# Kernel tuning notes

Measured on AMD Instinct MI355X. Metric: run time of the kernel, lower is better.

Reference implementation:

```python
import jax, jax.numpy as jnp
import numpy as np

N, M, E = 100000, 500, 300000
XS, GS, OUT, HEADS = 100, 100, 100, 2
SLOPE = 0.2
EPS = 1e-12


def l2norm(x, axis):
    n = jnp.linalg.norm(x, axis=axis, keepdims=True)
    return x / jnp.maximum(n, EPS)


def gat_layer(h_ijk, ends, n, W, att):
    # W: [heads*out, in_dim] (no bias); att: [1, heads, out]
    heads, out = att.shape[1], att.shape[2]
    c = (h_ijk @ W.T).reshape(-1, heads, out)               # [E, H, D]
    a = jnp.sum(att * c, axis=2, keepdims=True)             # [E, H, 1]
    e = jnp.exp(-jax.nn.leaky_relu(a, SLOPE))
    denom = jax.ops.segment_sum(e, ends, num_segments=n)    # [n, H, 1]
    alpha = e / denom[ends]                                 # segment softmax (dropout=eval/identity)
    h = jax.ops.segment_sum(alpha * c, ends, num_segments=n)  # [n, H, D]
    h = jax.nn.elu(h)
    h = l2norm(h, axis=2)
    return h.reshape(n, heads * out)


def merge_layer(h_in, h_out, Wi, bi, Wo, bo, Wl, bl):
    hi = h_in @ Wi.T + bi
    ho = h_out @ Wo.T + bo
    lam = jax.nn.sigmoid(jnp.concatenate([hi, ho], axis=1) @ Wl.T + bl)
    h = lam * hi + (1.0 - lam) * ho
    return l2norm(jax.nn.elu(h), axis=1)


def setup_inputs() -> dict:
    key = jax.random.key(0)
    ks = jax.random.split(key, 24)
    D = HEADS * OUT  # 200
    in1 = 2 * XS + GS   # 300
    in2 = 3 * D         # 600
    s = 0.05
    return {
        'edge_idx': jax.random.randint(ks[0], (2, E), 0, N),
        'edge_type': jax.random.randint(ks[1], (E,), 0, M),
        'path_idx': jax.random.randint(ks[2], (2, 8), 0, N),
        'path_type': jax.random.randint(ks[3], (2, 8), 0, M),
        'use_path': 0,
        'x': jax.random.normal(ks[4], (N, XS), jnp.float32),
        'g': jax.random.normal(ks[5], (M, GS), jnp.float32),
        'W_in1': s * jax.random.normal(ks[6], (D, in1), jnp.float32),
        'att_in1': s * jax.random.normal(ks[7], (1, HEADS, OUT), jnp.float32),
        'W_out1': s * jax.random.normal(ks[8], (D, in1), jnp.float32),
        'att_out1': s * jax.random.normal(ks[9], (1, HEADS, OUT), jnp.float32),
        'Wi1': s * jax.random.normal(ks[10], (D, D), jnp.float32), 'bi1': jnp.zeros((D,), jnp.float32),
        'Wo1': s * jax.random.normal(ks[11], (D, D), jnp.float32), 'bo1': jnp.zeros((D,), jnp.float32),
        'Wl1': s * jax.random.normal(ks[12], (1, 2 * D), jnp.float32), 'bl1': jnp.zeros((1,), jnp.float32),
        'Wr': s * jax.random.normal(ks[13], (D, GS), jnp.float32), 'br': jnp.zeros((D,), jnp.float32),
        'Wf': s * jax.random.normal(ks[14], (D, in1), jnp.float32), 'bf': jnp.zeros((D,), jnp.float32),
        'W_in2': s * jax.random.normal(ks[15], (D, in2), jnp.float32),
        'att_in2': s * jax.random.normal(ks[16], (1, 1, D), jnp.float32),
        'W_out2': s * jax.random.normal(ks[17], (D, in2), jnp.float32),
        'att_out2': s * jax.random.normal(ks[18], (1, 1, D), jnp.float32),
        'Wi2': s * jax.random.normal(ks[19], (D, D), jnp.float32), 'bi2': jnp.zeros((D,), jnp.float32),
        'Wo2': s * jax.random.normal(ks[20], (D, D), jnp.float32), 'bo2': jnp.zeros((D,), jnp.float32),
        'Wl2': s * jax.random.normal(ks[21], (1, 2 * D), jnp.float32), 'bl2': jnp.zeros((1,), jnp.float32),
        'W_ent': s * jax.random.normal(ks[22], (D, XS), jnp.float32),
    }


def reference(edge_idx, edge_type, path_idx, path_type, use_path, x, g,
              W_in1, att_in1, W_out1, att_out1, Wi1, bi1, Wo1, bo1, Wl1, bl1,
              Wr, br, Wf, bf,
              W_in2, att_in2, W_out2, att_out2, Wi2, bi2, Wo2, bo2, Wl2, bl2,
              W_ent):
    n, m = x.shape[0], g.shape[0]
    x = l2norm(x, axis=1)  # x_initial is renormalized each forward
    row, col = edge_idx[0], edge_idx[1]
    # hop 1: gather-concat per-edge features [E, 2*XS+GS]
    h_ijk = jnp.concatenate([x[row], x[col], g[edge_type]], axis=1)
    h_in = gat_layer(h_ijk, col, n, W_in1, att_in1)
    h_out = gat_layer(h_ijk, row, n, W_out1, att_out1)
    h = merge_layer(h_in, h_out, Wi1, bi1, Wo1, bo1, Wl1, bl1)
    # relation layer
    g_edges = jax.ops.segment_sum(h_ijk, edge_type, num_segments=m)
    g_edges = jax.nn.elu(l2norm(g_edges, axis=1))
    g_prime = (g @ Wr.T + br) + (g_edges @ Wf.T + bf)
    # hop 2
    h_ijk2 = jnp.concatenate([h[row], h[col], g_prime[edge_type]], axis=1)
    h_in2 = gat_layer(h_ijk2, col, n, W_in2, att_in2)
    h_out2 = gat_layer(h_ijk2, row, n, W_out2, att_out2)
    h = merge_layer(h_in2, h_out2, Wi2, bi2, Wo2, bo2, Wl2, bl2)
    # entity residual layer
    h_prime = x @ W_ent.T + h
    return h_prime
```

## Files before the change

### kernel.cpp

```cpp
#include <hip/hip_runtime.h>
#include <cstddef>
#include <cstdint>

#define WSLOPE 0.2f
#define WEPS 1e-12f

typedef __attribute__((ext_vector_type(8))) short bf16x8;
typedef __attribute__((ext_vector_type(4))) float f32x4;

__device__ __forceinline__ float waveSum(float v) {
#pragma unroll
    for (int off = 32; off > 0; off >>= 1) v += __shfl_xor(v, off, 64);
    return v;
}
__device__ __forceinline__ float rowSum16(float v) {
#pragma unroll
    for (int off = 8; off > 0; off >>= 1) v += __shfl_xor(v, off, 64);
    return v;
}
__device__ __forceinline__ float eluf(float v) { return v > 0.f ? v : expm1f(v); }
__device__ __forceinline__ short f2bf(float f) {
    union { float f; uint32_t u; } v; v.f = f;
    uint32_t r = v.u + 0x7FFF + ((v.u >> 16) & 1);
    return (short)(r >> 16);
}
__device__ __forceinline__ float bf2f(short s) {
    union { uint32_t u; float f; } v; v.u = ((uint32_t)(uint16_t)s) << 16;
    return v.f;
}

__global__ void k_nodeprep(const float* __restrict__ x, float* __restrict__ invn,
                           short* __restrict__ xnb,
                           const float* __restrict__ wai, const float* __restrict__ wao,
                           float* __restrict__ rdi, float* __restrict__ cdi,
                           float* __restrict__ rdo, float* __restrict__ cdo, int N) {
    int wid = blockIdx.x * 4 + (threadIdx.x >> 6);
    int lane = threadIdx.x & 63;
    if (wid >= N) return;
    const float* p = x + (size_t)wid * 100;
    float a0 = p[lane];
    float a1 = (lane < 36) ? p[lane + 64] : 0.f;
    float ss = waveSum(a0 * a0 + a1 * a1);
    float inv = 1.f / fmaxf(sqrtf(ss), WEPS);
    if (lane == 0) invn[wid] = inv;
    float f0 = a0 * inv, f1 = a1 * inv;
    short* xb = xnb + (size_t)wid * 112;
    xb[lane] = f2bf(f0);
    if (lane < 36) xb[64 + lane] = f2bf(f1);
    else if (lane < 48) xb[64 + lane] = 0;
#pragma unroll
    for (int h = 0; h < 2; ++h) {
        const float* wi = wai + h * 300;
        const float* wo = wao + h * 300;
        float ri = f0 * wi[lane] + f1 * wi[lane + 64];
        float ci = f0 * wi[100 + lane] + f1 * wi[100 + lane + 64];
        float ro = f0 * wo[lane] + f1 * wo[lane + 64];
        float co = f0 * wo[100 + lane] + f1 * wo[100 + lane + 64];
        ri = waveSum(ri); ci = waveSum(ci); ro = waveSum(ro); co = waveSum(co);
        if (lane == 0) { rdi[wid * 2 + h] = ri; cdi[wid * 2 + h] = ci; rdo[wid * 2 + h] = ro; cdo[wid * 2 + h] = co; }
    }
}

__global__ void k_gprep(const float* __restrict__ g, short* __restrict__ gbf,
                        short* __restrict__ gcomb,
                        const float* __restrict__ wai, const float* __restrict__ wao,
                        float* __restrict__ gdi, float* __restrict__ gdo, int M) {
    int m = blockIdx.x * 4 + (threadIdx.x >> 6);
    int lane = threadIdx.x & 63;
    if (m >= M) return;
    const float* gm = g + (size_t)m * 100;
    float v0 = gm[lane];
    float v1 = (lane < 36) ? gm[lane + 64] : 0.f;
    short b0 = f2bf(v0), b1 = (lane < 36) ? f2bf(v1) : (short)0;
    short* gb = gbf + (size_t)m * 112;
    gb[lane] = b0;
    if (lane < 48) gb[64 + lane] = (lane < 36) ? b1 : (short)0;
    short* gc = gcomb + (size_t)m * 448;
    gc[lane] = b0;
    gc[64 + lane] = b1;
    float s0 = v0 * wai[200 + lane];
    float s1 = v0 * wai[500 + lane];
    float s2 = v0 * wao[200 + lane];
    float s3 = v0 * wao[500 + lane];
    if (lane < 36) {
        s0 += v1 * wai[264 + lane]; s1 += v1 * wai[564 + lane];
        s2 += v1 * wao[264 + lane]; s3 += v1 * wao[564 + lane];
    }
    s0 = waveSum(s0); s1 = waveSum(s1); s2 = waveSum(s2); s3 = waveSum(s3);
    if (lane == 0) { gdi[m * 2] = s0; gdi[m * 2 + 1] = s1; gdo[m * 2] = s2; gdo[m * 2 + 1] = s3; }
}

__global__ void k_count(const int* __restrict__ keys, int* __restrict__ cnt, int n) {
    int i = blockIdx.x * 256 + threadIdx.x;
    if (i < n) atomicAdd(&cnt[keys[i]], 1);
}

#define SCAN_CHUNK 2048
__global__ void k_blocksum(const int* __restrict__ cnt, int* __restrict__ bsum, int n) {
    __shared__ int sh[256];
    int b = blockIdx.x, t = threadIdx.x;
    int base = b * SCAN_CHUNK;
    int s = 0;
    for (int i = t; i < SCAN_CHUNK; i += 256) { int idx = base + i; if (idx < n) s += cnt[idx]; }
    sh[t] = s; __syncthreads();
    for (int off = 128; off > 0; off >>= 1) { if (t < off) sh[t] += sh[t + off]; __syncthreads(); }
    if (t == 0) bsum[b] = sh[0];
}

__global__ void k_scanwrite(const int* __restrict__ cnt, const int* __restrict__ bsum,
                            int* __restrict__ offs, int* __restrict__ cur, int n, int nb) {
    __shared__ int sh[256];
    __shared__ int sbase;
    int b = blockIdx.x, t = threadIdx.x;
    if (t == 0) { int s = 0; for (int i = 0; i < b; ++i) s += bsum[i]; sbase = s; }
    __syncthreads();
    int base = b * SCAN_CHUNK;
    int loc[8]; int ts = 0;
#pragma unroll
    for (int i = 0; i < 8; ++i) { int idx = base + t * 8 + i; int v = (idx < n) ? cnt[idx] : 0; loc[i] = ts; ts += v; }
    sh[t] = ts; __syncthreads();
    for (int off = 1; off < 256; off <<= 1) {
        int v = (t >= off) ? sh[t - off] : 0;
        __syncthreads();
        sh[t] += v;
        __syncthreads();
    }
    int excl = (t == 0) ? 0 : sh[t - 1];
    int gbase = sbase + excl;
#pragma unroll
    for (int i = 0; i < 8; ++i) {
        int idx = base + t * 8 + i;
        if (idx < n) { offs[idx] = gbase + loc[i]; cur[idx] = gbase + loc[i]; }
    }
    if (b == nb - 1 && t == 255) offs[n] = sbase + sh[255];
}

__global__ void k_scatter3(const int* __restrict__ keys, const int* __restrict__ other,
                           const int* __restrict__ et, int* __restrict__ cur,
                           int* __restrict__ nbrS, int* __restrict__ etS,
                           int* __restrict__ keyS, int n) {
    int i = blockIdx.x * 256 + threadIdx.x;
    if (i < n) {
        int p = atomicAdd(&cur[keys[i]], 1);
        nbrS[p] = other[i];
        etS[p] = et[i];
        keyS[p] = keys[i];
    }
}

__global__ void k_scatter2(const int* __restrict__ keys, int* __restrict__ cur,
                           int* __restrict__ rs, int* __restrict__ cs,
                           const int* __restrict__ row, const int* __restrict__ col, int n) {
    int i = blockIdx.x * 256 + threadIdx.x;
    if (i < n) {
        int p = atomicAdd(&cur[keys[i]], 1);
        rs[p] = row[i];
        cs[p] = col[i];
    }
}

__global__ void k_watt(const float* __restrict__ att, const float* __restrict__ W,
                       float* __restrict__ wa, int H, int DH, int K) {
    int id = blockIdx.x * 256 + threadIdx.x;
    if (id >= H * K) return;
    int h = id / K, k = id % K;
    float s = 0.f;
    for (int j = 0; j < DH; ++j) s += att[h * DH + j] * W[(size_t)(h * DH + j) * K + k];
    wa[id] = s;
}

__global__ void k_ew2(const int* __restrict__ nbi, const int* __restrict__ kyi,
                      const int* __restrict__ eti,
                      const int* __restrict__ nbo, const int* __restrict__ kyo,
                      const int* __restrict__ eto,
                      const float* __restrict__ rdi, const float* __restrict__ cdi,
                      const float* __restrict__ rdo, const float* __restrict__ cdo,
                      const float* __restrict__ gdi, const float* __restrict__ gdo,
                      float* __restrict__ ewi, float* __restrict__ ewo, int E, int H) {
    int id = blockIdx.x * 256 + threadIdx.x;
    int tot = E * H;
    if (id >= 2 * tot) return;
    if (id < tot) {
        int p = id / H, h = id - p * H;
        float a = rdi[nbi[p] * H + h] + cdi[kyi[p] * H + h] + gdi[eti[p] * H + h];
        float lr = a > 0.f ? a : WSLOPE * a;
        ewi[id] = expf(-lr);
    } else {
        int id2 = id - tot;
        int p = id2 / H, h = id2 - p * H;
        float a = cdo[nbo[p] * H + h] + rdo[kyo[p] * H + h] + gdo[eto[p] * H + h];
        float lr = a > 0.f ? a : WSLOPE * a;
        ewo[id2] = expf(-lr);
    }
}

template<bool HOP2>
__global__ void k_agg(const int* __restrict__ offs, const int* __restrict__ nbrS,
                      const int* __restrict__ etS, const float* __restrict__ ewS,
                      const short* __restrict__ featB, const short* __restrict__ gB,
                      short* __restrict__ A, int n0, int n1) {
    constexpr int H = HOP2 ? 1 : 2;
    constexpr int LDA = HOP2 ? 672 : 576;
    constexpr int FW = HOP2 ? 224 : 112;
    constexpr int GW = HOP2 ? 224 : 112;
    int node = n0 + blockIdx.x * 4 + (threadIdx.x >> 6);
    int lane = threadIdx.x & 63;
    if (node >= n1) return;
    int o = offs[node];
    int deg = offs[node + 1] - o;
    float va[7];
#pragma unroll
    for (int m = 0; m < 7; ++m) va[m] = 0.f;
    if (deg > 0) {
        float s0 = 0.f, s1 = 0.f;
        for (int i = lane; i < deg; i += 64) {
            s0 += ewS[(size_t)(o + i) * H];
            if (H == 2) s1 += ewS[(size_t)(o + i) * H + 1];
        }
        s0 = waveSum(s0);
        float rd0 = 1.f / s0, rd1 = rd0;
        if (H == 2) { s1 = waveSum(s1); rd1 = 1.f / s1; }
        for (int j = 0; j < deg; ++j) {
            float a0 = ewS[(size_t)(o + j) * H] * rd0;
            float a1 = (H == 2) ? ewS[(size_t)(o + j) * H + 1] * rd1 : a0;
            int nbr = nbrS[o + j];
            int et = etS[o + j];
            const short* fr = featB + (size_t)nbr * FW;
            const short* gr = gB + (size_t)et * GW;
            if (!HOP2) {
#pragma unroll
                for (int m = 0; m < 7; ++m) {
                    int d = lane + m * 64;
                    if (d < 100) va[m] += a0 * bf2f(fr[d]);
                    else if (d < 200) va[m] += a1 * bf2f(fr[d - 100]);
                    else if (d < 300) va[m] += a0 * bf2f(gr[d - 200]);
                    else if (d < 400) va[m] += a1 * bf2f(gr[d - 300]);
                }
            } else {
#pragma unroll
                for (int m = 0; m < 7; ++m) {
                    int d = lane + m * 64;
                    if (d < 200) va[m] += a0 * bf2f(fr[d]);
                    else if (d < 424) va[m] += a0 * bf2f(gr[d - 200]);
                }
            }
        }
    }
    size_t rb = (size_t)(node - n0);
    short* Ar = A + rb * LDA;
    if (!HOP2) {
#pragma unroll
        for (int m = 0; m < 7; ++m) {
            int d = lane + m * 64;
            if (d < 400) {
                int col = d < 100 ? d : (d < 200 ? d + 12 : (d < 300 ? d + 24 : d + 36));
                Ar[col] = f2bf(va[m]);
            }
        }
        if (lane < 48) { int q = lane / 12; int rm = lane - q * 12; Ar[q * 112 + 100 + rm] = 0; }
        const short* sf = featB + (size_t)node * 112;
#pragma unroll
        for (int mm = 0; mm < 2; ++mm) {
            int k = lane + mm * 64;
            if (k < 128) Ar[448 + k] = (deg > 0 && k < 112) ? sf[k] : (short)0;
        }
    } else {
#pragma unroll
        for (int m = 0; m < 7; ++m) {
            int d = lane + m * 64;
            if (d < 424) Ar[d < 200 ? d : d + 24] = f2bf(va[m]);
        }
        if (lane < 24) Ar[200 + lane] = 0;
        const short* sf = featB + (size_t)node * 224;
#pragma unroll
        for (int mm = 0; mm < 4; ++mm) {
            int k = lane + mm * 64;
            if (k < 224) Ar[448 + k] = deg > 0 ? sf[k] : (short)0;
        }
    }
}

template<int KSTEPS, int H>
__launch_bounds__(256)
__global__ void k_mgemm_post(const short* __restrict__ A, const short* __restrict__ Wb,
                             short* __restrict__ post, int rows, int lda) {
    constexpr int LDW = KSTEPS * 32;
    const int t = threadIdx.x;
    const int wv = t >> 6, l = t & 63;
    const int lhi = l >> 4, llo = l & 15;
    const int rbase = blockIdx.x * 64 + wv * 16;
    f32x4 acc[13];
#pragma unroll
    for (int j = 0; j < 13; ++j) acc[j] = f32x4{0.f, 0.f, 0.f, 0.f};
    const short* arow = A + (size_t)(rbase + llo) * lda + lhi * 8;
#pragma unroll
    for (int kt = 0; kt < KSTEPS; ++kt) {
        bf16x8 a = *(const bf16x8*)(arow + kt * 32);
#pragma unroll
        for (int j = 0; j < 13; ++j) {
            bf16x8 b = *(const bf16x8*)(Wb + (size_t)(j * 16 + llo) * LDW + kt * 32 + lhi * 8);
            acc[j] = __builtin_amdgcn_mfma_f32_16x16x32_bf16(a, b, acc[j], 0, 0, 0);
        }
    }
    const int r0 = rbase + lhi * 4;
#pragma unroll
    for (int e = 0; e < 4; ++e) {
        int r = r0 + e;
        if (r >= rows) continue;
        float v[13];
        float s0 = 0.f, s1 = 0.f;
#pragma unroll
        for (int j = 0; j < 13; ++j) {
            int d = j * 16 + llo;
            if (d < 200) {
                float xv = eluf(acc[j][e]);
                v[j] = xv;
                if (H == 1 || d < 100) s0 += xv * xv; else s1 += xv * xv;
            }
        }
        s0 = rowSum16(s0);
        float inv0 = 1.f / fmaxf(sqrtf(s0), WEPS);
        float inv1 = inv0;
        if (H == 2) { s1 = rowSum16(s1); inv1 = 1.f / fmaxf(sqrtf(s1), WEPS); }
        short* pr = post + (size_t)r * 224;
#pragma unroll
        for (int j = 0; j < 13; ++j) {
            int d = j * 16 + llo;
            if (d < 200) pr[d] = f2bf(v[j] * ((H == 2 && d >= 100) ? inv1 : inv0));
        }
    }
}

template<bool HOP1>
__launch_bounds__(512)
__global__ void k_mergemm2(const short* __restrict__ pA, const short* __restrict__ pB,
                           const short* __restrict__ Wi, const short* __restrict__ Wo,
                           const float* __restrict__ bi, const float* __restrict__ bo,
                           const float* __restrict__ Wl, const float* __restrict__ bl,
                           const short* __restrict__ xnb, const short* __restrict__ Went,
                           float* __restrict__ outf, short* __restrict__ h1b,
                           const float* __restrict__ wa2i, const float* __restrict__ wa2o,
                           float* __restrict__ rdi, float* __restrict__ cdi,
                           float* __restrict__ rdo, float* __restrict__ cdo,
                           int rows) {
    __shared__ float lpS[2][64];
    __shared__ float ssS[2][64];
    __shared__ float dotS[2][64][4];
    const int t = threadIdx.x;
    const int wvAll = t >> 6;
    const int rg = wvAll >> 1;
    const int half = wvAll & 1;
    const int l = t & 63;
    const int lhi = l >> 4, llo = l & 15;
    const int jbase = half * 7;
    const int rbase = blockIdx.x * 64 + rg * 16;
    f32x4 accA[7], accB[7];
#pragma unroll
    for (int j = 0; j < 7; ++j) { accA[j] = f32x4{0.f, 0.f, 0.f, 0.f}; accB[j] = f32x4{0.f, 0.f, 0.f, 0.f}; }
    const short* pa = pA + (size_t)(rbase + llo) * 224 + lhi * 8;
    const short* pb = pB + (size_t)(rbase + llo) * 224 + lhi * 8;
#pragma unroll
    for (int kt = 0; kt < 7; ++kt) {
        bf16x8 a1 = *(const bf16x8*)(pa + kt * 32);
        bf16x8 a2 = *(const bf16x8*)(pb + kt * 32);
#pragma unroll
        for (int j = 0; j < 7; ++j) {
            if (jbase + j < 13) {
                bf16x8 b1 = *(const bf16x8*)(Wi + (size_t)((jbase + j) * 16 + llo) * 224 + kt * 32 + lhi * 8);
                accA[j] = __builtin_amdgcn_mfma_f32_16x16x32_bf16(a1, b1, accA[j], 0, 0, 0);
                bf16x8 b2 = *(const bf16x8*)(Wo + (size_t)((jbase + j) * 16 + llo) * 224 + kt * 32 + lhi * 8);
                accB[j] = __builtin_amdgcn_mfma_f32_16x16x32_bf16(a2, b2, accB[j], 0, 0, 0);
            }
        }
    }
    f32x4 accR[7];
    if (!HOP1) {
#pragma unroll
        for (int j = 0; j < 7; ++j) accR[j] = f32x4{0.f, 0.f, 0.f, 0.f};
        const short* xr = xnb + (size_t)(rbase + llo) * 112 + lhi * 8;
#pragma unroll
        for (int kt = 0; kt < 4; ++kt) {
            bf16x8 a = *(const bf16x8*)(xr + kt * 32);
#pragma unroll
            for (int j = 0; j < 7; ++j) {
                if (jbase + j < 13) {
                    bf16x8 b = *(const bf16x8*)(Went + (size_t)((jbase + j) * 16 + llo) * 128 + kt * 32 + lhi * 8);
                    accR[j] = __builtin_amdgcn_mfma_f32_16x16x32_bf16(a, b, accR[j], 0, 0, 0);
                }
            }
        }
    }
    const int r0 = rbase + lhi * 4;
    const int rrb = rg * 16 + lhi * 4;
    float blv = bl[0];
#pragma unroll
    for (int e = 0; e < 4; ++e) {
        float lp = 0.f;
#pragma unroll
        for (int j = 0; j < 7; ++j) {
            int d = (jbase + j) * 16 + llo;
            if (jbase + j < 13 && d < 200)
                lp += Wl[d] * (accA[j][e] + bi[d]) + Wl[200 + d] * (accB[j][e] + bo[d]);
        }
        lp = rowSum16(lp);
        if (llo == 0) lpS[half][rrb + e] = lp;
    }
    __syncthreads();
    float lamAll[4];
#pragma unroll
    for (int e = 0; e < 4; ++e) {
        float lam = 1.f / (1.f + expf(-(lpS[0][rrb + e] + lpS[1][rrb + e] + blv)));
        lamAll[e] = lam;
        float ss = 0.f;
#pragma unroll
        for (int j = 0; j < 7; ++j) {
            int d = (jbase + j) * 16 + llo;
            if (jbase + j < 13 && d < 200) {
                float vi = accA[j][e] + bi[d];
                float vo = accB[j][e] + bo[d];
                float hv = eluf(lam * vi + (1.f - lam) * vo);
                ss += hv * hv;
            }
        }
        ss = rowSum16(ss);
        if (llo == 0) ssS[half][rrb + e] = ss;
    }
    __syncthreads();
#pragma unroll
    for (int e = 0; e < 4; ++e) {
        int r = r0 + e;
        if (r >= rows) continue;
        float inv = 1.f / fmaxf(sqrtf(ssS[0][rrb + e] + ssS[1][rrb + e]), WEPS);
        float lam = lamAll[e];
        float ri = 0.f, ci = 0.f, ro = 0.f, co = 0.f;
#pragma unroll
        for (int j = 0; j < 7; ++j) {
            if (jbase + j >= 13) continue;
            int d = (jbase + j) * 16 + llo;
            if (d < 200) {
                float vi = accA[j][e] + bi[d];
                float vo = accB[j][e] + bo[d];
                float val = eluf(lam * vi + (1.f - lam) * vo) * inv;
                if (HOP1) {
                    h1b[(size_t)r * 224 + d] = f2bf(val);
                    ri += val * wa2i[d]; ci += val * wa2i[200 + d];
                    ro += val * wa2o[d]; co += val * wa2o[200 + d];
                } else {
                    outf[(size_t)r * 200 + d] = val + accR[j][e];
                }
            } else if (HOP1) {
                h1b[(size_t)r * 224 + d] = 0;
            }
        }
        if (HOP1) {
            if (half) h1b[(size_t)r * 224 + 208 + llo] = 0;
            ri = rowSum16(ri); ci = rowSum16(ci); ro = rowSum16(ro); co = rowSum16(co);
            if (llo == 0) {
                dotS[half][rrb + e][0] = ri; dotS[half][rrb + e][1] = ci;
                dotS[half][rrb + e][2] = ro; dotS[half][rrb + e][3] = co;
            }
        }
    }
    if (HOP1) {
        __syncthreads();
        if (half == 0 && llo == 0) {
#pragma unroll
            for (int e = 0; e < 4; ++e) {
                int r = r0 + e;
                if (r < rows) {
                    rdi[r] = dotS[0][rrb + e][0] + dotS[1][rrb + e][0];
                    cdi[r] = dotS[0][rrb + e][1] + dotS[1][rrb + e][1];
                    rdo[r] = dotS[0][rrb + e][2] + dotS[1][rrb + e][2];
                    cdo[r] = dotS[0][rrb + e][3] + dotS[1][rrb + e][3];
                }
            }
        }
    }
}

__launch_bounds__(256)
__global__ void k_mgemm_rel(const short* __restrict__ A, const short* __restrict__ Wb,
                            const float* __restrict__ brf,
                            short* __restrict__ gout, const float* __restrict__ wai,
                            const float* __restrict__ wao,
                            float* __restrict__ gdi, float* __restrict__ gdo, int rows) {
    constexpr int KSTEPS = 14, LDW = KSTEPS * 32;
    const int t = threadIdx.x;
    const int wv = t >> 6, l = t & 63;
    const int lhi = l >> 4, llo = l & 15;
    const int rbase = blockIdx.x * 64 + wv * 16;
    f32x4 acc[13];
#pragma unroll
    for (int j = 0; j < 13; ++j) acc[j] = f32x4{0.f, 0.f, 0.f, 0.f};
    const short* arow = A + (size_t)(rbase + llo) * 448 + lhi * 8;
#pragma unroll
    for (int kt = 0; kt < KSTEPS; ++kt) {
        bf16x8 a = *(const bf16x8*)(arow + kt * 32);
#pragma unroll
        for (int j = 0; j < 13; ++j) {
            bf16x8 b = *(const bf16x8*)(Wb + (size_t)(j * 16 + llo) * LDW + kt * 32 + lhi * 8);
            acc[j] = __builtin_amdgcn_mfma_f32_16x16x32_bf16(a, b, acc[j], 0, 0, 0);
        }
    }
    const int r0 = rbase + lhi * 4;
#pragma unroll
    for (int e = 0; e < 4; ++e) {
        int r = r0 + e;
        if (r >= rows) continue;
        short* pr = gout + (size_t)r * 224;
        float gi = 0.f, go = 0.f;
#pragma unroll
        for (int j = 0; j < 13; ++j) {
            int d = j * 16 + llo;
            if (d < 200) {
                float val = acc[j][e] + brf[d];
                pr[d] = f2bf(val);
                gi += val * wai[400 + d];
                go += val * wao[400 + d];
            } else {
                pr[d] = 0;
            }
        }
        pr[208 + llo] = 0;
        gi = rowSum16(gi); go = rowSum16(go);
        if (llo == 0) { gdi[r] = gi; gdo[r] = go; }
    }
}

__global__ void k_prepw(const float* __restrict__ W, int ldW, int koff, int Klen, int span,
                        int mode, short* __restrict__ Wb, int ldWb, int dst) {
    int id = blockIdx.x * 256 + threadIdx.x;
    int tot = 208 * span;
    if (id >= tot) return;
    int d = id / span, k = id - d * span;
    float v = 0.f;
    if (d < 200) {
        if (mode == 0) { if (k < Klen) v = W[(size_t)d * ldW + koff + k]; }
        else { int h = d / 100; int kk = k - h * 112; if (kk >= 0 && kk < Klen) v = W[(size_t)d * ldW + koff + kk]; }
    }
    Wb[(size_t)d * ldWb + dst + k] = f2bf(v);
}

__global__ void k_prepwrf(const float* __restrict__ Wr, const float* __restrict__ Wf,
                          short* __restrict__ Wb) {
    int id = blockIdx.x * 256 + threadIdx.x;
    if (id >= 208 * 448) return;
    int d = id / 448, k = id - d * 448;
    float v = 0.f;
    if (d < 200) {
        if (k < 100) v = Wr[(size_t)d * 100 + k];
        else if (k >= 128 && k < 428) v = Wf[(size_t)d * 300 + (k - 128)];
    }
    Wb[id] = f2bf(v);
}

__global__ void k_brf(const float* __restrict__ br, const float* __restrict__ bf,
                      float* __restrict__ brf) {
    int d = threadIdx.x;
    if (d < 200) brf[d] = br[d] + bf[d];
}

__global__ void k_gedges_b(const int* __restrict__ rsT, const int* __restrict__ csT,
                           const int* __restrict__ offsT,
                           const float* __restrict__ x, const float* __restrict__ invn,
                           const float* __restrict__ g, short* __restrict__ gcomb, int M) {
    __shared__ float red[6];
    int m = blockIdx.x, t = threadIdx.x;
    int o = offsT[m];
    int deg = offsT[m + 1] - o;
    float acc = 0.f;
    if (t < 128) {
        int d = t; bool ok = d < 100;
        for (int i = 0; i < deg; ++i) {
            int r = rsT[o + i];
            if (ok) acc += x[(size_t)r * 100 + d] * invn[r];
        }
    } else if (t < 256) {
        int d = t - 128; bool ok = d < 100;
        for (int i = 0; i < deg; ++i) {
            int c = csT[o + i];
            if (ok) acc += x[(size_t)c * 100 + d] * invn[c];
        }
    } else {
        int d = t - 256;
        if (d < 100) acc = (float)deg * g[(size_t)m * 100 + d];
    }
    float sq = waveSum(acc * acc);
    if ((t & 63) == 0) red[t >> 6] = sq;
    __syncthreads();
    float s2 = red[0] + red[1] + red[2] + red[3] + red[4] + red[5];
    float inv = 1.f / fmaxf(sqrtf(s2), WEPS);
    short* orow = gcomb + (size_t)m * 448 + 128;
    if (t < 128) {
        if (t < 100) orow[t] = f2bf(eluf(acc * inv));
    } else if (t < 256) {
        int d = t - 128;
        if (d < 100) orow[100 + d] = f2bf(eluf(acc * inv));
    } else {
        int d = t - 256;
        if (d < 100) orow[200 + d] = f2bf(eluf(acc * inv));
        else if (d < 120) orow[200 + d] = 0;
    }
}

extern "C" void kernel_launch(void* const* d_in, const int* in_sizes, int n_in,
                              void* d_out, int out_size, void* d_ws, size_t ws_size,
                              hipStream_t stream) {
    const int* eidx   = (const int*)d_in[0];
    const int* etype  = (const int*)d_in[1];
    const float* x    = (const float*)d_in[5];
    const float* g    = (const float*)d_in[6];
    const float* W_in1  = (const float*)d_in[7];
    const float* att_in1 = (const float*)d_in[8];
    const float* W_out1 = (const float*)d_in[9];
    const float* att_out1 = (const float*)d_in[10];
    const float* Wi1 = (const float*)d_in[11]; const float* bi1 = (const float*)d_in[12];
    const float* Wo1 = (const float*)d_in[13]; const float* bo1 = (const float*)d_in[14];
    const float* Wl1 = (const float*)d_in[15]; const float* bl1 = (const float*)d_in[16];
    const float* Wr  = (const float*)d_in[17]; const float* br  = (const float*)d_in[18];
    const float* Wf  = (const float*)d_in[19]; const float* bf  = (const float*)d_in[20];
    const float* W_in2  = (const float*)d_in[21]; const float* att_in2 = (const float*)d_in[22];
    const float* W_out2 = (const float*)d_in[23]; const float* att_out2 = (const float*)d_in[24];
    const float* Wi2 = (const float*)d_in[25]; const float* bi2 = (const float*)d_in[26];
    const float* Wo2 = (const float*)d_in[27]; const float* bo2 = (const float*)d_in[28];
    const float* Wl2 = (const float*)d_in[29]; const float* bl2 = (const float*)d_in[30];
    const float* W_ent = (const float*)d_in[31];

    const int E = in_sizes[1];
    const int N = in_sizes[5] / 100;
    const int M = in_sizes[6] / 100;
    const int Mr = (M + 63) & ~63;
    float* out = (float*)d_out;
    const int* row = eidx;
    const int* col = eidx + E;

    char* w = (char*)d_ws;
    size_t off_b = 0;
    auto alloc = [&](size_t bytes) -> void* {
        void* p = w + off_b;
        off_b += (bytes + 255) & ~(size_t)255;
        return p;
    };
    float* invn  = (float*)alloc((size_t)N * 4);
    short* h1_bf = (short*)alloc((size_t)(N + 64) * 224 * 2);
    short* xn_bf = (short*)alloc((size_t)(N + 64) * 112 * 2);
    short* g_bf  = (short*)alloc((size_t)M * 112 * 2);
    short* gp_bf = (short*)alloc((size_t)Mr * 224 * 2);
    int* offs_in = (int*)alloc((size_t)(N + 1) * 4);
    int* offs_out= (int*)alloc((size_t)(N + 1) * 4);
    int* offsT   = (int*)alloc((size_t)(M + 1) * 4);
    int* nbrS_in = (int*)alloc((size_t)E * 4);
    int* etS_in  = (int*)alloc((size_t)E * 4);
    int* keyS_in = (int*)alloc((size_t)E * 4);
    int* nbrS_out= (int*)alloc((size_t)E * 4);
    int* etS_out = (int*)alloc((size_t)E * 4);
    int* keyS_out= (int*)alloc((size_t)E * 4);
    int* rsT     = (int*)alloc((size_t)E * 4);
    int* csT     = (int*)alloc((size_t)E * 4);
    int* cnt     = (int*)alloc((size_t)N * 4);
    int* cur     = (int*)alloc((size_t)N * 4);
    int* bsum    = (int*)alloc((size_t)64 * 4);
    float* wa1_in = (float*)alloc((size_t)640 * 4);
    float* wa1_out= (float*)alloc((size_t)640 * 4);
    float* wa2_in = (float*)alloc((size_t)640 * 4);
    float* wa2_out= (float*)alloc((size_t)640 * 4);
    float* rdot_in = (float*)alloc((size_t)N * 2 * 4);
    float* cdot_in = (float*)alloc((size_t)N * 2 * 4);
    float* rdot_out= (float*)alloc((size_t)N * 2 * 4);
    float* cdot_out= (float*)alloc((size_t)N * 2 * 4);
    float* gdot_in = (float*)alloc((size_t)M * 2 * 4);
    float* gdot_out= (float*)alloc((size_t)M * 2 * 4);
    float* ewS_in  = (float*)alloc((size_t)E * 2 * 4);
    float* ewS_out = (float*)alloc((size_t)E * 2 * 4);
    short* gcomb   = (short*)alloc((size_t)Mr * 448 * 2);
    short* Wc_in1  = (short*)alloc((size_t)208 * 576 * 2);
    short* Wc_out1 = (short*)alloc((size_t)208 * 576 * 2);
    short* Wc_in2  = (short*)alloc((size_t)208 * 672 * 2);
    short* Wc_out2 = (short*)alloc((size_t)208 * 672 * 2);
    short* Wm_i1   = (short*)alloc((size_t)208 * 224 * 2);
    short* Wm_o1   = (short*)alloc((size_t)208 * 224 * 2);
    short* Wm_i2   = (short*)alloc((size_t)208 * 224 * 2);
    short* Wm_o2   = (short*)alloc((size_t)208 * 224 * 2);
    short* Wb_ent  = (short*)alloc((size_t)208 * 128 * 2);
    short* Wrf_b   = (short*)alloc((size_t)208 * 448 * 2);
    float* brf     = (float*)alloc((size_t)200 * 4);

    if (off_b >= ws_size) return;
    size_t rem = ws_size - off_b;
    long long Cll = (long long)(rem / 3712);
    long long Nr64 = ((long long)N + 63) & ~63LL;
    int C = (int)(Cll > Nr64 ? Nr64 : Cll);
    C &= ~63;
    if (C < 64) return;
    short* Ac0   = (short*)alloc((size_t)C * 672 * 2);
    short* Ac1   = (short*)alloc((size_t)C * 672 * 2);
    short* postA = (short*)alloc((size_t)C * 224 * 2);
    short* postB = (short*)alloc((size_t)C * 224 * 2);
    if (off_b > ws_size) return;

    const int gE = (E + 255) / 256;
    const int gN4 = (N + 3) / 4;
    const int gM4 = (M + 3) / 4;
    const int gM64 = (M + 63) / 64;

    hipMemsetAsync(postA, 0, (size_t)C * 224 * 2, stream);
    hipMemsetAsync(postB, 0, (size_t)C * 224 * 2, stream);

    auto gsp = [](int span) { return (208 * span + 255) / 256; };
    k_prepw<<<gsp(224), 256, 0, stream>>>(W_in1, 300, 0, 100, 224, 1, Wc_in1, 576, 0);
    k_prepw<<<gsp(224), 256, 0, stream>>>(W_in1, 300, 200, 100, 224, 1, Wc_in1, 576, 224);
    k_prepw<<<gsp(128), 256, 0, stream>>>(W_in1, 300, 100, 100, 128, 0, Wc_in1, 576, 448);
    k_prepw<<<gsp(224), 256, 0, stream>>>(W_out1, 300, 100, 100, 224, 1, Wc_out1, 576, 0);
    k_prepw<<<gsp(224), 256, 0, stream>>>(W_out1, 300, 200, 100, 224, 1, Wc_out1, 576, 224);
    k_prepw<<<gsp(128), 256, 0, stream>>>(W_out1, 300, 0, 100, 128, 0, Wc_out1, 576, 448);
    k_prepw<<<gsp(224), 256, 0, stream>>>(W_in2, 600, 0, 200, 224, 0, Wc_in2, 672, 0);
    k_prepw<<<gsp(224), 256, 0, stream>>>(W_in2, 600, 400, 200, 224, 0, Wc_in2, 672, 224);
    k_prepw<<<gsp(224), 256, 0, stream>>>(W_in2, 600, 200, 200, 224, 0, Wc_in2, 672, 448);
    k_prepw<<<gsp(224), 256, 0, stream>>>(W_out2, 600, 200, 200, 224, 0, Wc_out2, 672, 0);
    k_prepw<<<gsp(224), 256, 0, stream>>>(W_out2, 600, 400, 200, 224, 0, Wc_out2, 672, 224);
    k_prepw<<<gsp(224), 256, 0, stream>>>(W_out2, 600, 0, 200, 224, 0, Wc_out2, 672, 448);
    k_prepw<<<gsp(224), 256, 0, stream>>>(Wi1, 200, 0, 200, 224, 0, Wm_i1, 224, 0);
    k_prepw<<<gsp(224), 256, 0, stream>>>(Wo1, 200, 0, 200, 224, 0, Wm_o1, 224, 0);
    k_prepw<<<gsp(224), 256, 0, stream>>>(Wi2, 200, 0, 200, 224, 0, Wm_i2, 224, 0);
    k_prepw<<<gsp(224), 256, 0, stream>>>(Wo2, 200, 0, 200, 224, 0, Wm_o2, 224, 0);
    k_prepw<<<gsp(128), 256, 0, stream>>>(W_ent, 100, 0, 100, 128, 0, Wb_ent, 128, 0);
    k_prepwrf<<<gsp(448), 256, 0, stream>>>(Wr, Wf, Wrf_b);
    k_brf<<<1, 256, 0, stream>>>(br, bf, brf);

    int nbN = (N + SCAN_CHUNK - 1) / SCAN_CHUNK;
    int nbM = (M + SCAN_CHUNK - 1) / SCAN_CHUNK;
    hipMemsetAsync(cnt, 0, (size_t)N * 4, stream);
    k_count<<<gE, 256, 0, stream>>>(col, cnt, E);
    k_blocksum<<<nbN, 256, 0, stream>>>(cnt, bsum, N);
    k_scanwrite<<<nbN, 256, 0, stream>>>(cnt, bsum, offs_in, cur, N, nbN);
    k_scatter3<<<gE, 256, 0, stream>>>(col, row, etype, cur, nbrS_in, etS_in, keyS_in, E);

    hipMemsetAsync(cnt, 0, (size_t)N * 4, stream);
    k_count<<<gE, 256, 0, stream>>>(row, cnt, E);
    k_blocksum<<<nbN, 256, 0, stream>>>(cnt, bsum, N);
    k_scanwrite<<<nbN, 256, 0, stream>>>(cnt, bsum, offs_out, cur, N, nbN);
    k_scatter3<<<gE, 256, 0, stream>>>(row, col, etype, cur, nbrS_out, etS_out, keyS_out, E);

    hipMemsetAsync(cnt, 0, (size_t)M * 4, stream);
    k_count<<<gE, 256, 0, stream>>>(etype, cnt, E);
    k_blocksum<<<nbM, 256, 0, stream>>>(cnt, bsum, M);
    k_scanwrite<<<nbM, 256, 0, stream>>>(cnt, bsum, offsT, cur, M, nbM);
    k_scatter2<<<gE, 256, 0, stream>>>(etype, cur, rsT, csT, row, col, E);

    k_watt<<<(600 + 255) / 256, 256, 0, stream>>>(att_in1, W_in1, wa1_in, 2, 100, 300);
    k_watt<<<(600 + 255) / 256, 256, 0, stream>>>(att_out1, W_out1, wa1_out, 2, 100, 300);
    k_watt<<<(600 + 255) / 256, 256, 0, stream>>>(att_in2, W_in2, wa2_in, 1, 200, 600);
    k_watt<<<(600 + 255) / 256, 256, 0, stream>>>(att_out2, W_out2, wa2_out, 1, 200, 600);

    k_nodeprep<<<gN4, 256, 0, stream>>>(x, invn, xn_bf, wa1_in, wa1_out,
                                        rdot_in, cdot_in, rdot_out, cdot_out, N);
    k_gprep<<<gM4, 256, 0, stream>>>(g, g_bf, gcomb, wa1_in, wa1_out, gdot_in, gdot_out, M);
    k_ew2<<<(2 * E * 2 + 255) / 256, 256, 0, stream>>>(nbrS_in, keyS_in, etS_in,
                                                       nbrS_out, keyS_out, etS_out,
                                                       rdot_in, cdot_in, rdot_out, cdot_out,
                                                       gdot_in, gdot_out, ewS_in, ewS_out, E, 2);

    for (int n0 = 0; n0 < N; n0 += C) {
        int rows = (N - n0 < C) ? (N - n0) : C;
        int n1 = n0 + rows;
        int ga = (rows + 3) / 4;
        int gb = (rows + 63) / 64;
        k_agg<false><<<ga, 256, 0, stream>>>(offs_in, nbrS_in, etS_in, ewS_in, xn_bf, g_bf, Ac0, n0, n1);
        k_agg<false><<<ga, 256, 0, stream>>>(offs_out, nbrS_out, etS_out, ewS_out, xn_bf, g_bf, Ac1, n0, n1);
        k_mgemm_post<18, 2><<<gb, 256, 0, stream>>>(Ac0, Wc_in1, postA, rows, 576);
        k_mgemm_post<18, 2><<<gb, 256, 0, stream>>>(Ac1, Wc_out1, postB, rows, 576);
        k_mergemm2<true><<<gb, 512, 0, stream>>>(postA, postB, Wm_i1, Wm_o1, bi1, bo1, Wl1, bl1,
                                                 nullptr, nullptr,
                                                 nullptr, h1_bf + (size_t)n0 * 224,
                                                 wa2_in, wa2_out,
                                                 rdot_in + n0, cdot_in + n0,
                                                 rdot_out + n0, cdot_out + n0, rows);
    }

    k_gedges_b<<<M, 384, 0, stream>>>(rsT, csT, offsT, x, invn, g, gcomb, M);
    k_mgemm_rel<<<gM64, 256, 0, stream>>>(gcomb, Wrf_b, brf, gp_bf, wa2_in, wa2_out, gdot_in, gdot_out, M);

    k_ew2<<<(2 * E + 255) / 256, 256, 0, stream>>>(nbrS_in, keyS_in, etS_in,
                                                   nbrS_out, keyS_out, etS_out,
                                                   rdot_in, cdot_in, rdot_out, cdot_out,
                                                   gdot_in, gdot_out, ewS_in, ewS_out, E, 1);

    for (int n0 = 0; n0 < N; n0 += C) {
        int rows = (N - n0 < C) ? (N - n0) : C;
        int n1 = n0 + rows;
        int ga = (rows + 3) / 4;
        int gb = (rows + 63) / 64;
        k_agg<true><<<ga, 256, 0, stream>>>(offs_in, nbrS_in, etS_in, ewS_in, h1_bf, gp_bf, Ac0, n0, n1);
        k_agg<true><<<ga, 256, 0, stream>>>(offs_out, nbrS_out, etS_out, ewS_out, h1_bf, gp_bf, Ac1, n0, n1);
        k_mgemm_post<21, 1><<<gb, 256, 0, stream>>>(Ac0, Wc_in2, postA, rows, 672);
        k_mgemm_post<21, 1><<<gb, 256, 0, stream>>>(Ac1, Wc_out2, postB, rows, 672);
        k_mergemm2<false><<<gb, 512, 0, stream>>>(postA, postB, Wm_i2, Wm_o2, bi2, bo2, Wl2, bl2,
                                                  xn_bf + (size_t)n0 * 112, Wb_ent,
                                                  out + (size_t)n0 * 200, nullptr,
                                                  nullptr, nullptr,
                                                  nullptr, nullptr, nullptr, nullptr, rows);
    }
}
```

Baseline: 2.535 ms.

## Read self features directly in GEMM instead of copying into staging buffer

```diff
diff --git a/kernel.cpp b/kernel.cpp
--- a/kernel.cpp
+++ b/kernel.cpp
@@ -75,9 +75,9 @@
     short* gb = gbf + (size_t)m * 112;
     gb[lane] = b0;
     if (lane < 48) gb[64 + lane] = (lane < 36) ? b1 : (short)0;
-    short* gc = gcomb + (size_t)m * 448;
+    short* gc = gcomb + (size_t)m * 416;
     gc[lane] = b0;
-    gc[64 + lane] = b1;
+    if (lane < 48) gc[64 + lane] = (lane < 36) ? b1 : (short)0;
     float s0 = v0 * wai[200 + lane];
     float s1 = v0 * wai[500 + lane];
     float s2 = v0 * wao[200 + lane];
@@ -200,7 +200,7 @@
                       const short* __restrict__ featB, const short* __restrict__ gB,
                       short* __restrict__ A, int n0, int n1) {
     constexpr int H = HOP2 ? 1 : 2;
-    constexpr int LDA = HOP2 ? 672 : 576;
+    constexpr int LDA = 448;
     constexpr int FW = HOP2 ? 224 : 112;
     constexpr int GW = HOP2 ? 224 : 112;
     int node = n0 + blockIdx.x * 4 + (threadIdx.x >> 6);
@@ -258,12 +258,6 @@
             }
         }
         if (lane < 48) { int q = lane / 12; int rm = lane - q * 12; Ar[q * 112 + 100 + rm] = 0; }
-        const short* sf = featB + (size_t)node * 112;
-#pragma unroll
-        for (int mm = 0; mm < 2; ++mm) {
-            int k = lane + mm * 64;
-            if (k < 128) Ar[448 + k] = (deg > 0 && k < 112) ? sf[k] : (short)0;
-        }
     } else {
 #pragma unroll
         for (int m = 0; m < 7; ++m) {
@@ -271,34 +265,45 @@
             if (d < 424) Ar[d < 200 ? d : d + 24] = f2bf(va[m]);
         }
         if (lane < 24) Ar[200 + lane] = 0;
-        const short* sf = featB + (size_t)node * 224;
-#pragma unroll
-        for (int mm = 0; mm < 4; ++mm) {
-            int k = lane + mm * 64;
-            if (k < 224) Ar[448 + k] = deg > 0 ? sf[k] : (short)0;
-        }
-    }
-}
-
-template<int KSTEPS, int H>
+    }
+}
+
+template<int KS_S, int H>
 __launch_bounds__(256)
 __global__ void k_mgemm_post(const short* __restrict__ A, const short* __restrict__ Wb,
-                             short* __restrict__ post, int rows, int lda) {
-    constexpr int LDW = KSTEPS * 32;
+                             const short* __restrict__ selfB, int selfLD,
+                             const int* __restrict__ offs,
+                             short* __restrict__ post, int rows) {
+    constexpr int KS_A = 14;
+    constexpr int LDW = (KS_A + KS_S) * 32;
     const int t = threadIdx.x;
     const int wv = t >> 6, l = t & 63;
     const int lhi = l >> 4, llo = l & 15;
     const int rbase = blockIdx.x * 64 + wv * 16;
+    const int ra = rbase + llo;
+    const int deg = (ra < rows) ? (offs[ra + 1] - offs[ra]) : 0;
     f32x4 acc[13];
 #pragma unroll
     for (int j = 0; j < 13; ++j) acc[j] = f32x4{0.f, 0.f, 0.f, 0.f};
-    const short* arow = A + (size_t)(rbase + llo) * lda + lhi * 8;
-#pragma unroll
-    for (int kt = 0; kt < KSTEPS; ++kt) {
+    const short* arow = A + (size_t)ra * 448 + lhi * 8;
+#pragma unroll
+    for (int kt = 0; kt < KS_A; ++kt) {
         bf16x8 a = *(const bf16x8*)(arow + kt * 32);
 #pragma unroll
         for (int j = 0; j < 13; ++j) {
             bf16x8 b = *(const bf16x8*)(Wb + (size_t)(j * 16 + llo) * LDW + kt * 32 + lhi * 8);
+            acc[j] = __builtin_amdgcn_mfma_f32_16x16x32_bf16(a, b, acc[j], 0, 0, 0);
+        }
+    }
+    const short* srow = selfB + (size_t)ra * selfLD + lhi * 8;
+#pragma unroll
+    for (int kt = 0; kt < KS_S; ++kt) {
+        bf16x8 a;
+        if (deg > 0) a = *(const bf16x8*)(srow + kt * 32);
+        else a = bf16x8{0, 0, 0, 0, 0, 0, 0, 0};
+#pragma unroll
+        for (int j = 0; j < 13; ++j) {
+            bf16x8 b = *(const bf16x8*)(Wb + (size_t)(j * 16 + llo) * LDW + (KS_A + kt) * 32 + lhi * 8);
             acc[j] = __builtin_amdgcn_mfma_f32_16x16x32_bf16(a, b, acc[j], 0, 0, 0);
         }
     }
@@ -484,7 +489,7 @@
                             short* __restrict__ gout, const float* __restrict__ wai,
                             const float* __restrict__ wao,
                             float* __restrict__ gdi, float* __restrict__ gdo, int rows) {
-    constexpr int KSTEPS = 14, LDW = KSTEPS * 32;
+    constexpr int KSTEPS = 13, LDW = KSTEPS * 32;
     const int t = threadIdx.x;
     const int wv = t >> 6, l = t & 63;
     const int lhi = l >> 4, llo = l & 15;
@@ -492,7 +497,7 @@
     f32x4 acc[13];
 #pragma unroll
     for (int j = 0; j < 13; ++j) acc[j] = f32x4{0.f, 0.f, 0.f, 0.f};
-    const short* arow = A + (size_t)(rbase + llo) * 448 + lhi * 8;
+    const short* arow = A + (size_t)(rbase + llo) * 416 + lhi * 8;
 #pragma unroll
     for (int kt = 0; kt < KSTEPS; ++kt) {
         bf16x8 a = *(const bf16x8*)(arow + kt * 32);
@@ -544,12 +549,12 @@
 __global__ void k_prepwrf(const float* __restrict__ Wr, const float* __restrict__ Wf,
                           short* __restrict__ Wb) {
     int id = blockIdx.x * 256 + threadIdx.x;
-    if (id >= 208 * 448) return;
-    int d = id / 448, k = id - d * 448;
+    if (id >= 208 * 416) return;
+    int d = id / 416, k = id - d * 416;
     float v = 0.f;
     if (d < 200) {
         if (k < 100) v = Wr[(size_t)d * 100 + k];
-        else if (k >= 128 && k < 428) v = Wf[(size_t)d * 300 + (k - 128)];
+        else if (k >= 112 && k < 412) v = Wf[(size_t)d * 300 + (k - 112)];
     }
     Wb[id] = f2bf(v);
 }
@@ -563,7 +568,7 @@
 __global__ void k_gedges_b(const int* __restrict__ rsT, const int* __restrict__ csT,
                            const int* __restrict__ offsT,
                            const float* __restrict__ x, const float* __restrict__ invn,
-                           const float* __restrict__ g, short* __restrict__ gcomb, int M) {
+                           const short* __restrict__ gbf, short* __restrict__ gcomb, int M) {
     __shared__ float red[6];
     int m = blockIdx.x, t = threadIdx.x;
     int o = offsT[m];
@@ -583,14 +588,14 @@
         }
     } else {
         int d = t - 256;
-        if (d < 100) acc = (float)deg * g[(size_t)m * 100 + d];
+        if (d < 100) acc = (float)deg * bf2f(gbf[(size_t)m * 112 + d]);
     }
     float sq = waveSum(acc * acc);
     if ((t & 63) == 0) red[t >> 6] = sq;
     __syncthreads();
     float s2 = red[0] + red[1] + red[2] + red[3] + red[4] + red[5];
     float inv = 1.f / fmaxf(sqrtf(s2), WEPS);
-    short* orow = gcomb + (size_t)m * 448 + 128;
+    short* orow = gcomb + (size_t)m * 416 + 112;
     if (t < 128) {
         if (t < 100) orow[t] = f2bf(eluf(acc * inv));
     } else if (t < 256) {
@@ -599,7 +604,7 @@
     } else {
         int d = t - 256;
         if (d < 100) orow[200 + d] = f2bf(eluf(acc * inv));
-        else if (d < 120) orow[200 + d] = 0;
+        else if (d < 104) orow[200 + d] = 0;
     }
 }
 
@@ -672,7 +677,7 @@
     float* gdot_out= (float*)alloc((size_t)M * 2 * 4);
     float* ewS_in  = (float*)alloc((size_t)E * 2 * 4);
     float* ewS_out = (float*)alloc((size_t)E * 2 * 4);
-    short* gcomb   = (short*)alloc((size_t)Mr * 448 * 2);
+    short* gcomb   = (short*)alloc((size_t)Mr * 416 * 2);
     short* Wc_in1  = (short*)alloc((size_t)208 * 576 * 2);
     short* Wc_out1 = (short*)alloc((size_t)208 * 576 * 2);
     short* Wc_in2  = (short*)alloc((size_t)208 * 672 * 2);
@@ -682,18 +687,18 @@
     short* Wm_i2   = (short*)alloc((size_t)208 * 224 * 2);
     short* Wm_o2   = (short*)alloc((size_t)208 * 224 * 2);
     short* Wb_ent  = (short*)alloc((size_t)208 * 128 * 2);
-    short* Wrf_b   = (short*)alloc((size_t)208 * 448 * 2);
+    short* Wrf_b   = (short*)alloc((size_t)208 * 416 * 2);
     float* brf     = (float*)alloc((size_t)200 * 4);
 
     if (off_b >= ws_size) return;
     size_t rem = ws_size - off_b;
-    long long Cll = (long long)(rem / 3712);
+    long long Cll = (long long)(rem / 1920);
     long long Nr64 = ((long long)N + 63) & ~63LL;
+    if (Cll > 32768) Cll = 32768;
     int C = (int)(Cll > Nr64 ? Nr64 : Cll);
     C &= ~63;
     if (C < 64) return;
-    short* Ac0   = (short*)alloc((size_t)C * 672 * 2);
-    short* Ac1   = (short*)alloc((size_t)C * 672 * 2);
+    short* Ac    = (short*)alloc((size_t)C * 448 * 2);
     short* postA = (short*)alloc((size_t)C * 224 * 2);
     short* postB = (short*)alloc((size_t)C * 224 * 2);
     if (off_b > ws_size) return;
@@ -705,6 +710,8 @@
 
     hipMemsetAsync(postA, 0, (size_t)C * 224 * 2, stream);
     hipMemsetAsync(postB, 0, (size_t)C * 224 * 2, stream);
+    hipMemsetAsync(xn_bf + (size_t)N * 112, 0, (size_t)64 * 112 * 2, stream);
+    hipMemsetAsync(h1_bf + (size_t)N * 224, 0, (size_t)64 * 224 * 2, stream);
 
     auto gsp = [](int span) { return (208 * span + 255) / 256; };
     k_prepw<<<gsp(224), 256, 0, stream>>>(W_in1, 300, 0, 100, 224, 1, Wc_in1, 576, 0);
@@ -724,7 +731,7 @@
     k_prepw<<<gsp(224), 256, 0, stream>>>(Wi2, 200, 0, 200, 224, 0, Wm_i2, 224, 0);
     k_prepw<<<gsp(224), 256, 0, stream>>>(Wo2, 200, 0, 200, 224, 0, Wm_o2, 224, 0);
     k_prepw<<<gsp(128), 256, 0, stream>>>(W_ent, 100, 0, 100, 128, 0, Wb_ent, 128, 0);
-    k_prepwrf<<<gsp(448), 256, 0, stream>>>(Wr, Wf, Wrf_b);
+    k_prepwrf<<<gsp(416), 256, 0, stream>>>(Wr, Wf, Wrf_b);
     k_brf<<<1, 256, 0, stream>>>(br, bf, brf);
 
     int nbN = (N + SCAN_CHUNK - 1) / SCAN_CHUNK;
@@ -765,10 +772,12 @@
         int n1 = n0 + rows;
         int ga = (rows + 3) / 4;
         int gb = (rows + 63) / 64;
-        k_agg<false><<<ga, 256, 0, stream>>>(offs_in, nbrS_in, etS_in, ewS_in, xn_bf, g_bf, Ac0, n0, n1);
-        k_agg<false><<<ga, 256, 0, stream>>>(offs_out, nbrS_out, etS_out, ewS_out, xn_bf, g_bf, Ac1, n0, n1);
-        k_mgemm_post<18, 2><<<gb, 256, 0, stream>>>(Ac0, Wc_in1, postA, rows, 576);
-        k_mgemm_post<18, 2><<<gb, 256, 0, stream>>>(Ac1, Wc_out1, postB, rows, 576);
+        k_agg<false><<<ga, 256, 0, stream>>>(offs_in, nbrS_in, etS_in, ewS_in, xn_bf, g_bf, Ac, n0, n1);
+        k_mgemm_post<4, 2><<<gb, 256, 0, stream>>>(Ac, Wc_in1, xn_bf + (size_t)n0 * 112, 112,
+                                                   offs_in + n0, postA, rows);
+        k_agg<false><<<ga, 256, 0, stream>>>(offs_out, nbrS_out, etS_out, ewS_out, xn_bf, g_bf, Ac, n0, n1);
+        k_mgemm_post<4, 2><<<gb, 256, 0, stream>>>(Ac, Wc_out1, xn_bf + (size_t)n0 * 112, 112,
+                                                   offs_out + n0, postB, rows);
         k_mergemm2<true><<<gb, 512, 0, stream>>>(postA, postB, Wm_i1, Wm_o1, bi1, bo1, Wl1, bl1,
                                                  nullptr, nullptr,
                                                  nullptr, h1_bf + (size_t)n0 * 224,
@@ -777,7 +786,7 @@
                                                  rdot_out + n0, cdot_out + n0, rows);
     }
 
-    k_gedges_b<<<M, 384, 0, stream>>>(rsT, csT, offsT, x, invn, g, gcomb, M);
+    k_gedges_b<<<M, 384, 0, stream>>>(rsT, csT, offsT, x, invn, g_bf, gcomb, M);
     k_mgemm_rel<<<gM64, 256, 0, stream>>>(gcomb, Wrf_b, brf, gp_bf, wa2_in, wa2_out, gdot_in, gdot_out, M);
 
     k_ew2<<<(2 * E + 255) / 256, 256, 0, stream>>>(nbrS_in, keyS_in, etS_in,
@@ -790,10 +799,12 @@
         int n1 = n0 + rows;
         int ga = (rows + 3) / 4;
         int gb = (rows + 63) / 64;
-        k_agg<true><<<ga, 256, 0, stream>>>(offs_in, nbrS_in, etS_in, ewS_in, h1_bf, gp_bf, Ac0, n0, n1);
-        k_agg<true><<<ga, 256, 0, stream>>>(offs_out, nbrS_out, etS_out, ewS_out, h1_bf, gp_bf, Ac1, n0, n1);
-        k_mgemm_post<21, 1><<<gb, 256, 0, stream>>>(Ac0, Wc_in2, postA, rows, 672);
-        k_mgemm_post<21, 1><<<gb, 256, 0, stream>>>(Ac1, Wc_out2, postB, rows, 672);
+        k_agg<true><<<ga, 256, 0, stream>>>(offs_in, nbrS_in, etS_in, ewS_in, h1_bf, gp_bf, Ac, n0, n1);
+        k_mgemm_post<7, 1><<<gb, 256, 0, stream>>>(Ac, Wc_in2, h1_bf + (size_t)n0 * 224, 224,
+                                                   offs_in + n0, postA, rows);
+        k_agg<true><<<ga, 256, 0, stream>>>(offs_out, nbrS_out, etS_out, ewS_out, h1_bf, gp_bf, Ac, n0, n1);
+        k_mgemm_post<7, 1><<<gb, 256, 0, stream>>>(Ac, Wc_out2, h1_bf + (size_t)n0 * 224, 224,
+                                                   offs_out + n0, postB, rows);
         k_mergemm2<false><<<gb, 512, 0, stream>>>(postA, postB, Wm_i2, Wm_o2, bi2, bo2, Wl2, bl2,
                                                   xn_bf + (size_t)n0 * 112, Wb_ent,
                                                   out + (size_t)n0 * 200, nullptr,
```

After: 2.842 ms. +12.1%, slower.
